# Kernel optimization log

Measured on AMD Instinct MI355X. Metric: run time of the kernel, lower is better.

Reference implementation:

```python
import jax, jax.numpy as jnp
import numpy as np
from jax.ops import segment_sum

N = 100000
E = 1600000
D_IN = 64
D_H = 64
D_OUT = 16


def _gcn_norm(edge_index, n_nodes):
    # PyG GCNConv default: add self-loops, symmetric normalization.
    src, dst = edge_index[0], edge_index[1]
    loop = jnp.arange(n_nodes, dtype=edge_index.dtype)
    src = jnp.concatenate([src, loop])
    dst = jnp.concatenate([dst, loop])
    deg = segment_sum(jnp.ones(src.shape[0], dtype=jnp.float32), dst, num_segments=n_nodes)
    dinv = jnp.where(deg > 0, jax.lax.rsqrt(deg), 0.0)
    norm = dinv[src] * dinv[dst]  # [E + N]
    return src, dst, norm


def _gcn_layer(x, W, b, src, dst, norm, n_nodes):
    h = x @ W  # dense transform first (out_channels <= in_channels)
    msg = h[src] * norm[:, None]          # gather + scale  [E+N, out]
    agg = segment_sum(msg, dst, num_segments=n_nodes)  # scatter-add
    return agg + b


def setup_inputs() -> dict:
    key = jax.random.key(0)
    ks = jax.random.split(key, 10)
    x = jax.random.normal(ks[0], (N, D_IN), dtype=jnp.float32)
    edge_index = jax.random.randint(ks[1], (2, E), 0, N, dtype=jnp.int64)

    def glorot(k, fan_in, fan_out):
        lim = np.sqrt(6.0 / (fan_in + fan_out)).astype(np.float32)
        return jax.random.uniform(k, (fan_in, fan_out), jnp.float32, -lim, lim)

    return {
        "x": x,
        "edge_index": edge_index,
        "W1": glorot(ks[2], D_IN, D_H), "b1": jnp.zeros((D_H,), jnp.float32),
        "W2": glorot(ks[3], D_H, D_H), "b2": jnp.zeros((D_H,), jnp.float32),
        "W3": glorot(ks[4], D_H, D_H), "b3": jnp.zeros((D_H,), jnp.float32),
        "W4": glorot(ks[5], D_H, D_OUT), "b4": jnp.zeros((D_OUT,), jnp.float32),
    }


def reference(x, edge_index, W1, b1, W2, b2, W3, b3, W4, b4):
    n = x.shape[0]
    src, dst, norm = _gcn_norm(edge_index, n)
    h = jax.nn.relu(_gcn_layer(x, W1, b1, src, dst, norm, n))
    h = jax.nn.relu(_gcn_layer(h, W2, b2, src, dst, norm, n))
    h = jax.nn.relu(_gcn_layer(h, W3, b3, src, dst, norm, n))
    return _gcn_layer(h, W4, b4, src, dst, norm, n)
```

## Files before the change

kernel.cpp:

```cpp
#include <hip/hip_runtime.h>
#include <hip/hip_fp16.h>

#define NN 100000
#define NE 1600000
#define BK 512
#define BKSH 9
#define NBKT 196
#define SLOT 9216
#define SRCMASK 0x1FFFF

typedef _Float16 half2v __attribute__((ext_vector_type(2)));

__device__ inline float dot2acc(unsigned int a, unsigned int b, float c) {
#if __has_builtin(__builtin_amdgcn_fdot2)
    union { unsigned int u; half2v h; } ua, ub;
    ua.u = a; ub.u = b;
    return __builtin_amdgcn_fdot2(ua.h, ub.h, c, false);
#else
    float2 fa = __half22float2(*(const __half2*)&a);
    float2 fb = __half22float2(*(const __half2*)&b);
    return c + fa.x * fb.x + fa.y * fb.y;
#endif
}

__device__ inline int wave_incl_scan(int v, int lane) {
#pragma unroll
    for (int off = 1; off < 64; off <<= 1) {
        int t = __shfl_up(v, off, 64);
        if (lane >= off) v += t;
    }
    return v;
}


__global__ __launch_bounds__(256) void zero_small_kernel(int* __restrict__ p, int n) {
    int i = threadIdx.x + blockIdx.x * 256;
    if (i < n) p[i] = 0;
}

__global__ __launch_bounds__(512) void bscatter_kernel(const int* __restrict__ src,
                                                       const int* __restrict__ dst,
                                                       int* __restrict__ bcur,
                                                       unsigned int* __restrict__ bedges,
                                                       int e) {
    __shared__ int h[256];
    __shared__ int sc[256];
    __shared__ int gb[256];
    __shared__ int2 stg[4096];
    int tid = threadIdx.x;
    int tile = blockIdx.x * 4096;
    int cnt_tile = min(4096, e - tile);
    if (tid < 256) h[tid] = 0;
    __syncthreads();
    unsigned int pk[8]; int rk[8], bk[8];
#pragma unroll
    for (int j = 0; j < 8; j++) {
        int li = tid + j * 512;
        if (li < cnt_tile) {
            int s = src[tile + li];
            int d = dst[tile + li];
            bk[j] = d >> BKSH;
            pk[j] = ((unsigned)(d & (BK - 1)) << 17) | (unsigned)s;
            rk[j] = atomicAdd(&h[bk[j]], 1);
        } else bk[j] = -1;
    }
    __syncthreads();
    if (tid < 64) {
        int b0 = tid * 4;
        int c0 = h[b0], c1 = h[b0 + 1], c2 = h[b0 + 2], c3 = h[b0 + 3];
        int s4 = c0 + c1 + c2 + c3;
        int incl = wave_incl_scan(s4, tid);
        int base = incl - s4;
        sc[b0] = base; sc[b0 + 1] = base + c0;
        sc[b0 + 2] = base + c0 + c1; sc[b0 + 3] = base + c0 + c1 + c2;
        if (c0) gb[b0] = atomicAdd(&bcur[b0], c0);
        if (c1) gb[b0 + 1] = atomicAdd(&bcur[b0 + 1], c1);
        if (c2) gb[b0 + 2] = atomicAdd(&bcur[b0 + 2], c2);
        if (c3) gb[b0 + 3] = atomicAdd(&bcur[b0 + 3], c3);
    }
    __syncthreads();
#pragma unroll
    for (int j = 0; j < 8; j++)
        if (bk[j] >= 0) stg[sc[bk[j]] + rk[j]] = make_int2((int)pk[j], bk[j]);
    __syncthreads();
#pragma unroll
    for (int j = 0; j < 8; j++) {
        int li = tid + j * 512;
        if (li < cnt_tile) {
            int2 p2 = stg[li];
            int b = p2.y;
            bedges[(size_t)b * SLOT + gb[b] + (li - sc[b])] = (unsigned int)p2.x;
        }
    }
}

__global__ __launch_bounds__(1024) void bfill_kernel(const unsigned int* __restrict__ bedges,
                                                     const int* __restrict__ bcur,
                                                     int* __restrict__ start,
                                                     int* __restrict__ cnt,
                                                     float* __restrict__ dinv,
                                                     int* __restrict__ csr) {
    __shared__ int lcnt[BK];
    __shared__ int lstart[BK];
    __shared__ int lcur[BK];
    int q = blockIdx.x, tid = threadIdx.x;
    size_t ebase = (size_t)q * SLOT;
    int ec = bcur[q];
    int nbase = q * BK;
    if (tid < BK) lcnt[tid] = 0;
    __syncthreads();
    for (int i = tid; i < ec; i += 1024)
        atomicAdd(&lcnt[__builtin_nontemporal_load(&bedges[ebase + i]) >> 17], 1);
    __syncthreads();
    if (tid < 64) {
        int b0 = tid * 8;
        int c[8]; int s = 0;
#pragma unroll
        for (int k = 0; k < 8; k++) { c[k] = lcnt[b0 + k]; s += c[k]; }
        int incl = wave_incl_scan(s, tid);
        int run = incl - s;
#pragma unroll
        for (int k = 0; k < 8; k++) { lstart[b0 + k] = run; lcur[b0 + k] = run; run += c[k]; }
    }
    __syncthreads();
    if (tid < BK) {
        int nd = nbase + tid;
        if (nd < NN) {
            start[nd] = (int)ebase + lstart[tid];
            cnt[nd]   = lcnt[tid];
            dinv[nd]  = rsqrtf((float)lcnt[tid] + 1.0f);
        }
    }
    for (int i = tid; i < ec; i += 1024) {
        unsigned int pk = __builtin_nontemporal_load(&bedges[ebase + i]);
        int r = atomicAdd(&lcur[pk >> 17], 1);
        csr[ebase + r] = (int)(pk & SRCMASK);
    }
}

__global__ __launch_bounds__(256) void prep_kernel(const float* __restrict__ x,
                                                   const float* __restrict__ dinv,
                                                   __half* __restrict__ g) {
    size_t i4 = (size_t)blockIdx.x * 256 + threadIdx.x;
    if (i4 >= (size_t)NN * 16) return;
    int row = (int)(i4 >> 4);
    float dv = dinv[row];
    float4 v = *(const float4*)&x[i4 * 4];
    __half2 h01 = __floats2half2_rn(v.x * dv, v.y * dv);
    __half2 h23 = __floats2half2_rn(v.z * dv, v.w * dv);
    __half2* gp = (__half2*)&g[i4 * 4];
    gp[0] = h01;
    gp[1] = h23;
}

__global__ __launch_bounds__(512) void fused_layer_kernel(const __half* __restrict__ g,
                                                          const int* __restrict__ csr,
                                                          const int* __restrict__ start,
                                                          const int* __restrict__ cnt,
                                                          const float* __restrict__ dinv,
                                                          const float* __restrict__ Wg,
                                                          const float* __restrict__ bias,
                                                          __half* __restrict__ gout, int n) {
    __shared__ uint4 wpk[8][64];
    __shared__ __half zh[8][64];
    __shared__ float bs[64];
    int tid = threadIdx.x;
    {
        int p = tid >> 6, c = tid & 63;
        float w[8];
#pragma unroll
        for (int i = 0; i < 8; i++) w[i] = Wg[(8 * p + i) * 64 + c];
        union { __half2 h; unsigned int u; } u0, u1, u2, u3;
        u0.h = __floats2half2_rn(w[0], w[1]);
        u1.h = __floats2half2_rn(w[2], w[3]);
        u2.h = __floats2half2_rn(w[4], w[5]);
        u3.h = __floats2half2_rn(w[6], w[7]);
        wpk[p][c] = make_uint4(u0.u, u1.u, u2.u, u3.u);
    }
    if (tid < 64) bs[tid] = bias[tid];
    __syncthreads();

    int wv = tid >> 6, lane = tid & 63;
    int node = blockIdx.x * 8 + wv;
    float acc = 0.f;
    float dv = 0.f;
    if (node < n) {
        int st = __builtin_amdgcn_readfirstlane(start[node]);
        int cn = __builtin_amdgcn_readfirstlane(cnt[node]);
        dv = dinv[node];
        acc = __half2float(g[(size_t)node * 64 + lane]);
        int e = 0;
        for (; e + 7 < cn; e += 8) {
            int u[8]; float a[8];
#pragma unroll
            for (int j = 0; j < 8; j++) u[j] = __builtin_nontemporal_load(&csr[st + e + j]);
#pragma unroll
            for (int j = 0; j < 8; j++) a[j] = __half2float(g[(size_t)u[j] * 64 + lane]);
            acc += ((a[0] + a[1]) + (a[2] + a[3])) + ((a[4] + a[5]) + (a[6] + a[7]));
        }
        for (; e + 3 < cn; e += 4) {
            int u0 = __builtin_nontemporal_load(&csr[st + e + 0]);
            int u1 = __builtin_nontemporal_load(&csr[st + e + 1]);
            int u2 = __builtin_nontemporal_load(&csr[st + e + 2]);
            int u3 = __builtin_nontemporal_load(&csr[st + e + 3]);
            float a0 = __half2float(g[(size_t)u0 * 64 + lane]);
            float a1 = __half2float(g[(size_t)u1 * 64 + lane]);
            float a2 = __half2float(g[(size_t)u2 * 64 + lane]);
            float a3 = __half2float(g[(size_t)u3 * 64 + lane]);
            acc += (a0 + a1) + (a2 + a3);
        }
        for (; e < cn; e++) {
            int u = __builtin_nontemporal_load(&csr[st + e]);
            acc += __half2float(g[(size_t)u * 64 + lane]);
        }
    }
    zh[wv][lane] = __float2half_rn(acc);
    if (node < n) {
        float t = 0.f;
#pragma unroll
        for (int p = 0; p < 8; p++) {
            uint4 wq = wpk[p][lane];
            uint4 zq = *(const uint4*)&zh[wv][p * 8];
            t = dot2acc(zq.x, wq.x, t);
            t = dot2acc(zq.y, wq.y, t);
            t = dot2acc(zq.z, wq.z, t);
            t = dot2acc(zq.w, wq.w, t);
        }
        float o = dv * t + bs[lane];
        o = fmaxf(o, 0.f);
        gout[(size_t)node * 64 + lane] = __float2half_rn(dv * o);
    }
}

__global__ __launch_bounds__(128) void gemm16_kernel(const __half* __restrict__ xin,
                                                     const float* __restrict__ W,
                                                     __half* __restrict__ s, int n) {
    constexpr int DOUT = 16;
    constexpr int ROWS = 128;
    __shared__ float xs[ROWS][65];
    __shared__ float ws[64][DOUT];
    int tid = threadIdx.x;
    int row0 = blockIdx.x * ROWS;
    for (int i = tid; i < 64 * DOUT; i += 128) ws[i / DOUT][i % DOUT] = W[i];
    for (int i = tid; i < ROWS * 16; i += 128) {
        int r = i >> 4, c = (i & 15) * 4;
        float4 v = make_float4(0.f, 0.f, 0.f, 0.f);
        if (row0 + r < n) {
            const __half* hp = xin + (size_t)(row0 + r) * 64 + c;
            float2 f01 = __half22float2(*(const __half2*)hp);
            float2 f23 = __half22float2(*(const __half2*)(hp + 2));
            v = make_float4(f01.x, f01.y, f23.x, f23.y);
        }
        xs[r][c] = v.x; xs[r][c + 1] = v.y; xs[r][c + 2] = v.z; xs[r][c + 3] = v.w;
    }
    __syncthreads();
    int rbase = tid;
    float acc[16];
#pragma unroll
    for (int j = 0; j < 16; j++) acc[j] = 0.f;
    for (int k = 0; k < 64; k++) {
        float xv = xs[rbase][k];
#pragma unroll
        for (int j = 0; j < 4; j++) {
            float4 wv = *(const float4*)&ws[k][j * 4];
            acc[j * 4 + 0] += xv * wv.x;
            acc[j * 4 + 1] += xv * wv.y;
            acc[j * 4 + 2] += xv * wv.z;
            acc[j * 4 + 3] += xv * wv.w;
        }
    }
    int r = row0 + rbase;
    if (r < n) {
        union { ushort u[16]; uint4 q[2]; } pk;
#pragma unroll
        for (int j = 0; j < 16; j++)
            pk.u[j] = __half_as_ushort(__float2half_rn(acc[j]));
        uint4* sp = (uint4*)&s[(size_t)r * DOUT];
        sp[0] = pk.q[0];
        sp[1] = pk.q[1];
    }
}

__global__ __launch_bounds__(256) void agg16_kernel(const __half* __restrict__ s,
                                                    const int* __restrict__ csr,
                                                    const int* __restrict__ start,
                                                    const int* __restrict__ cnt,
                                                    const float* __restrict__ dinv,
                                                    const float* __restrict__ bias,
                                                    float* __restrict__ out, int n) {
    constexpr int D = 16;
    int tid = threadIdx.x;
    int lane = tid & 63;
    int wave = tid >> 6;
    int col = lane % D;
    int grp = lane / D;
    int node = (blockIdx.x * 4 + wave) * 4 + grp;
    if (node >= n) return;
    int st = start[node];
    int cn = cnt[node];
    float acc = __half2float(s[(size_t)node * D + col]);
    int e = 0;
    for (; e + 7 < cn; e += 8) {
        int u[8]; float a[8];
#pragma unroll
        for (int j = 0; j < 8; j++) u[j] = __builtin_nontemporal_load(&csr[st + e + j]);
#pragma unroll
        for (int j = 0; j < 8; j++) a[j] = __half2float(s[(size_t)u[j] * D + col]);
        acc += ((a[0] + a[1]) + (a[2] + a[3])) + ((a[4] + a[5]) + (a[6] + a[7]));
    }
    for (; e + 3 < cn; e += 4) {
        int u0 = __builtin_nontemporal_load(&csr[st + e + 0]);
        int u1 = __builtin_nontemporal_load(&csr[st + e + 1]);
        int u2 = __builtin_nontemporal_load(&csr[st + e + 2]);
        int u3 = __builtin_nontemporal_load(&csr[st + e + 3]);
        float a0 = __half2float(s[(size_t)u0 * D + col]);
        float a1 = __half2float(s[(size_t)u1 * D + col]);
        float a2 = __half2float(s[(size_t)u2 * D + col]);
        float a3 = __half2float(s[(size_t)u3 * D + col]);
        acc += (a0 + a1) + (a2 + a3);
    }
    for (; e < cn; e++) {
        int u = __builtin_nontemporal_load(&csr[st + e]);
        acc += __half2float(s[(size_t)u * D + col]);
    }
    float o = dinv[node] * acc + bias[col];
    __builtin_nontemporal_store(o, out + (size_t)node * D + col);
}


extern "C" void kernel_launch(void* const* d_in, const int* in_sizes, int n_in,
                              void* d_out, int out_size, void* d_ws, size_t ws_size,
                              hipStream_t stream) {
    const float* x  = (const float*)d_in[0];
    const int* ei   = (const int*)d_in[1];
    const float* W1 = (const float*)d_in[2];
    const float* b1 = (const float*)d_in[3];
    const float* W2 = (const float*)d_in[4];
    const float* b2 = (const float*)d_in[5];
    const float* W3 = (const float*)d_in[6];
    const float* b3 = (const float*)d_in[7];
    const float* W4 = (const float*)d_in[8];
    const float* b4 = (const float*)d_in[9];
    const int* src = ei;
    const int* dst = ei + NE;

    char* w = (char*)d_ws;
    float* dinv  = (float*)w;          w += (size_t)NN * 4;
    int* cnt     = (int*)w;            w += (size_t)NN * 4;
    int* start   = (int*)w;            w += (size_t)NN * 4;
    int* bcur    = (int*)w;            w += (size_t)256 * 4;
    int* csr     = (int*)w;            w += (size_t)NBKT * SLOT * 4;
    __half* gA   = (__half*)w;         w += (size_t)NN * 64 * 2;
    __half* gB   = (__half*)w;         w += (size_t)NN * 64 * 2;
    __half* s4   = (__half*)w;         w += (size_t)NN * 16 * 2;
    unsigned int* bedges = (unsigned int*)w;  w += (size_t)NBKT * SLOT * 4;

    zero_small_kernel<<<1, 256, 0, stream>>>(bcur, 256);
    bscatter_kernel<<<(NE + 4095) / 4096, 512, 0, stream>>>(src, dst, bcur, bedges, NE);
    bfill_kernel<<<NBKT, 1024, 0, stream>>>(bedges, bcur, start, cnt, dinv, csr);

    prep_kernel<<<(NN * 16 + 255) / 256, 256, 0, stream>>>(x, dinv, gA);

    const int FB = (NN + 7) / 8;
    fused_layer_kernel<<<FB, 512, 0, stream>>>(gA, csr, start, cnt, dinv, W1, b1, gB, NN);
    fused_layer_kernel<<<FB, 512, 0, stream>>>(gB, csr, start, cnt, dinv, W2, b2, gA, NN);
    fused_layer_kernel<<<FB, 512, 0, stream>>>(gA, csr, start, cnt, dinv, W3, b3, gB, NN);

    const int GB = (NN + 127) / 128;
    const int AB16 = (NN + 15) / 16;
    gemm16_kernel<<<GB, 128, 0, stream>>>(gB, W4, s4, NN);
    agg16_kernel<<<AB16, 256, 0, stream>>>(s4, csr, start, cnt, dinv, b4, (float*)d_out, NN);
}
```

Baseline: 338.0 us.

## Process two nodes per wave in fused layer and stage bucket fill in LDS

The fused GCN layer kernel now gives each wavefront two destination nodes and interleaves their neighbor gathers, so more independent memory loads are in flight per wave. Block count is halved to match. Separately, bfill keeps the bucket's edges in registers instead of reading them from global memory twice, and builds the CSR slice in a shared-memory buffer before writing it out in a coalesced pass. The costs are higher register and LDS use (a 36KB sbuf), which may lower occupancy, plus duplicated code paths for the tails. The gather relies on each bucket holding at most 9216 edges, the existing SLOT size.

```diff
diff --git a/kernel.cpp b/kernel.cpp
--- a/kernel.cpp
+++ b/kernel.cpp
@@ -103,14 +103,22 @@
     __shared__ int lcnt[BK];
     __shared__ int lstart[BK];
     __shared__ int lcur[BK];
+    __shared__ unsigned int sbuf[SLOT];
     int q = blockIdx.x, tid = threadIdx.x;
     size_t ebase = (size_t)q * SLOT;
     int ec = bcur[q];
     int nbase = q * BK;
     if (tid < BK) lcnt[tid] = 0;
     __syncthreads();
-    for (int i = tid; i < ec; i += 1024)
-        atomicAdd(&lcnt[__builtin_nontemporal_load(&bedges[ebase + i]) >> 17], 1);
+    unsigned int pk[9];
+#pragma unroll
+    for (int k = 0; k < 9; k++) {
+        int i = tid + k * 1024;
+        pk[k] = (i < ec) ? __builtin_nontemporal_load(&bedges[ebase + i]) : 0xFFFFFFFFu;
+    }
+#pragma unroll
+    for (int k = 0; k < 9; k++)
+        if (pk[k] != 0xFFFFFFFFu) atomicAdd(&lcnt[pk[k] >> 17], 1);
     __syncthreads();
     if (tid < 64) {
         int b0 = tid * 8;
@@ -131,11 +139,16 @@
             dinv[nd]  = rsqrtf((float)lcnt[tid] + 1.0f);
         }
     }
-    for (int i = tid; i < ec; i += 1024) {
-        unsigned int pk = __builtin_nontemporal_load(&bedges[ebase + i]);
-        int r = atomicAdd(&lcur[pk >> 17], 1);
-        csr[ebase + r] = (int)(pk & SRCMASK);
-    }
+#pragma unroll
+    for (int k = 0; k < 9; k++) {
+        if (pk[k] != 0xFFFFFFFFu) {
+            int r = atomicAdd(&lcur[pk[k] >> 17], 1);
+            sbuf[r] = pk[k] & SRCMASK;
+        }
+    }
+    __syncthreads();
+    for (int i = tid; i < ec; i += 1024)
+        csr[ebase + i] = (int)sbuf[i];
 }
 
 __global__ __launch_bounds__(256) void prep_kernel(const float* __restrict__ x,
@@ -181,41 +194,102 @@
     __syncthreads();
 
     int wv = tid >> 6, lane = tid & 63;
-    int node = blockIdx.x * 8 + wv;
-    float acc = 0.f;
-    float dv = 0.f;
-    if (node < n) {
-        int st = __builtin_amdgcn_readfirstlane(start[node]);
-        int cn = __builtin_amdgcn_readfirstlane(cnt[node]);
-        dv = dinv[node];
-        acc = __half2float(g[(size_t)node * 64 + lane]);
-        int e = 0;
-        for (; e + 7 < cn; e += 8) {
-            int u[8]; float a[8];
-#pragma unroll
-            for (int j = 0; j < 8; j++) u[j] = __builtin_nontemporal_load(&csr[st + e + j]);
-#pragma unroll
-            for (int j = 0; j < 8; j++) a[j] = __half2float(g[(size_t)u[j] * 64 + lane]);
-            acc += ((a[0] + a[1]) + (a[2] + a[3])) + ((a[4] + a[5]) + (a[6] + a[7]));
-        }
-        for (; e + 3 < cn; e += 4) {
-            int u0 = __builtin_nontemporal_load(&csr[st + e + 0]);
-            int u1 = __builtin_nontemporal_load(&csr[st + e + 1]);
-            int u2 = __builtin_nontemporal_load(&csr[st + e + 2]);
-            int u3 = __builtin_nontemporal_load(&csr[st + e + 3]);
-            float a0 = __half2float(g[(size_t)u0 * 64 + lane]);
-            float a1 = __half2float(g[(size_t)u1 * 64 + lane]);
-            float a2 = __half2float(g[(size_t)u2 * 64 + lane]);
-            float a3 = __half2float(g[(size_t)u3 * 64 + lane]);
-            acc += (a0 + a1) + (a2 + a3);
-        }
-        for (; e < cn; e++) {
-            int u = __builtin_nontemporal_load(&csr[st + e]);
-            acc += __half2float(g[(size_t)u * 64 + lane]);
-        }
-    }
-    zh[wv][lane] = __float2half_rn(acc);
-    if (node < n) {
+    int nodeA = blockIdx.x * 16 + wv * 2;
+    int nodeB = nodeA + 1;
+
+    float accA = 0.f, accB = 0.f;
+    float dvA = 0.f, dvB = 0.f;
+    int stA = 0, cnA = 0, stB = 0, cnB = 0;
+    if (nodeA < n) {
+        stA = __builtin_amdgcn_readfirstlane(start[nodeA]);
+        cnA = __builtin_amdgcn_readfirstlane(cnt[nodeA]);
+        dvA = dinv[nodeA];
+        accA = __half2float(g[(size_t)nodeA * 64 + lane]);
+    }
+    if (nodeB < n) {
+        stB = __builtin_amdgcn_readfirstlane(start[nodeB]);
+        cnB = __builtin_amdgcn_readfirstlane(cnt[nodeB]);
+        dvB = dinv[nodeB];
+        accB = __half2float(g[(size_t)nodeB * 64 + lane]);
+    }
+
+    int eA = 0, eB = 0;
+    while (eA + 8 <= cnA && eB + 8 <= cnB) {
+        int uA[8], uB[8];
+#pragma unroll
+        for (int j = 0; j < 8; j++) uA[j] = __builtin_nontemporal_load(&csr[stA + eA + j]);
+#pragma unroll
+        for (int j = 0; j < 8; j++) uB[j] = __builtin_nontemporal_load(&csr[stB + eB + j]);
+        float aA[8], aB[8];
+#pragma unroll
+        for (int j = 0; j < 8; j++) aA[j] = __half2float(g[(size_t)uA[j] * 64 + lane]);
+#pragma unroll
+        for (int j = 0; j < 8; j++) aB[j] = __half2float(g[(size_t)uB[j] * 64 + lane]);
+        accA += ((aA[0] + aA[1]) + (aA[2] + aA[3])) + ((aA[4] + aA[5]) + (aA[6] + aA[7]));
+        accB += ((aB[0] + aB[1]) + (aB[2] + aB[3])) + ((aB[4] + aB[5]) + (aB[6] + aB[7]));
+        eA += 8; eB += 8;
+    }
+    for (; eA + 7 < cnA; eA += 8) {
+        int u[8]; float a[8];
+#pragma unroll
+        for (int j = 0; j < 8; j++) u[j] = __builtin_nontemporal_load(&csr[stA + eA + j]);
+#pragma unroll
+        for (int j = 0; j < 8; j++) a[j] = __half2float(g[(size_t)u[j] * 64 + lane]);
+        accA += ((a[0] + a[1]) + (a[2] + a[3])) + ((a[4] + a[5]) + (a[6] + a[7]));
+    }
+    for (; eB + 7 < cnB; eB += 8) {
+        int u[8]; float a[8];
+#pragma unroll
+        for (int j = 0; j < 8; j++) u[j] = __builtin_nontemporal_load(&csr[stB + eB + j]);
+#pragma unroll
+        for (int j = 0; j < 8; j++) a[j] = __half2float(g[(size_t)u[j] * 64 + lane]);
+        accB += ((a[0] + a[1]) + (a[2] + a[3])) + ((a[4] + a[5]) + (a[6] + a[7]));
+    }
+    if (eA + 3 < cnA && eB + 3 < cnB) {
+        int uA[4], uB[4];
+#pragma unroll
+        for (int j = 0; j < 4; j++) uA[j] = __builtin_nontemporal_load(&csr[stA + eA + j]);
+#pragma unroll
+        for (int j = 0; j < 4; j++) uB[j] = __builtin_nontemporal_load(&csr[stB + eB + j]);
+        float aA[4], aB[4];
+#pragma unroll
+        for (int j = 0; j < 4; j++) aA[j] = __half2float(g[(size_t)uA[j] * 64 + lane]);
+#pragma unroll
+        for (int j = 0; j < 4; j++) aB[j] = __half2float(g[(size_t)uB[j] * 64 + lane]);
+        accA += (aA[0] + aA[1]) + (aA[2] + aA[3]);
+        accB += (aB[0] + aB[1]) + (aB[2] + aB[3]);
+        eA += 4; eB += 4;
+    } else {
+        if (eA + 3 < cnA) {
+            int u[4]; float a[4];
+#pragma unroll
+            for (int j = 0; j < 4; j++) u[j] = __builtin_nontemporal_load(&csr[stA + eA + j]);
+#pragma unroll
+            for (int j = 0; j < 4; j++) a[j] = __half2float(g[(size_t)u[j] * 64 + lane]);
+            accA += (a[0] + a[1]) + (a[2] + a[3]);
+            eA += 4;
+        }
+        if (eB + 3 < cnB) {
+            int u[4]; float a[4];
+#pragma unroll
+            for (int j = 0; j < 4; j++) u[j] = __builtin_nontemporal_load(&csr[stB + eB + j]);
+#pragma unroll
+            for (int j = 0; j < 4; j++) a[j] = __half2float(g[(size_t)u[j] * 64 + lane]);
+            accB += (a[0] + a[1]) + (a[2] + a[3]);
+            eB += 4;
+        }
+    }
+    for (; eA < cnA; eA++) {
+        int u = __builtin_nontemporal_load(&csr[stA + eA]);
+        accA += __half2float(g[(size_t)u * 64 + lane]);
+    }
+    for (; eB < cnB; eB++) {
+        int u = __builtin_nontemporal_load(&csr[stB + eB]);
+        accB += __half2float(g[(size_t)u * 64 + lane]);
+    }
+
+    zh[wv][lane] = __float2half_rn(accA);
+    if (nodeA < n) {
         float t = 0.f;
 #pragma unroll
         for (int p = 0; p < 8; p++) {
@@ -226,9 +300,25 @@
             t = dot2acc(zq.z, wq.z, t);
             t = dot2acc(zq.w, wq.w, t);
         }
-        float o = dv * t + bs[lane];
+        float o = dvA * t + bs[lane];
         o = fmaxf(o, 0.f);
-        gout[(size_t)node * 64 + lane] = __float2half_rn(dv * o);
+        gout[(size_t)nodeA * 64 + lane] = __float2half_rn(dvA * o);
+    }
+    zh[wv][lane] = __float2half_rn(accB);
+    if (nodeB < n) {
+        float t = 0.f;
+#pragma unroll
+        for (int p = 0; p < 8; p++) {
+            uint4 wq = wpk[p][lane];
+            uint4 zq = *(const uint4*)&zh[wv][p * 8];
+            t = dot2acc(zq.x, wq.x, t);
+            t = dot2acc(zq.y, wq.y, t);
+            t = dot2acc(zq.z, wq.z, t);
+            t = dot2acc(zq.w, wq.w, t);
+        }
+        float o = dvB * t + bs[lane];
+        o = fmaxf(o, 0.f);
+        gout[(size_t)nodeB * 64 + lane] = __float2half_rn(dvB * o);
     }
 }
 
@@ -361,7 +451,7 @@
 
     prep_kernel<<<(NN * 16 + 255) / 256, 256, 0, stream>>>(x, dinv, gA);
 
-    const int FB = (NN + 7) / 8;
+    const int FB = (NN + 15) / 16;
     fused_layer_kernel<<<FB, 512, 0, stream>>>(gA, csr, start, cnt, dinv, W1, b1, gB, NN);
     fused_layer_kernel<<<FB, 512, 0, stream>>>(gB, csr, start, cnt, dinv, W2, b2, gA, NN);
     fused_layer_kernel<<<FB, 512, 0, stream>>>(gA, csr, start, cnt, dinv, W3, b3, gB, NN);
```

Measured after the change: 368.0 us. 1.09x slower.
